# Performance work log

Hardware: AMD Instinct MI355X
Metric: run time of the kernel (lower is better)

The kernel has to match this reference:

```python
import jax, jax.numpy as jnp
import numpy as np

H, U = 64, 64  # matrix-completion patch size; system size is (H*U)^2 = 4096^2


def svtC(X, tau):
    # Singular value thresholding: soft-threshold singular values by tau.
    u, s, vt = jnp.linalg.svd(X, full_matrices=False)
    return (u * jax.nn.relu(s - tau)) @ vt


def setup_inputs() -> dict:
    key = jax.random.key(0)
    ks = jax.random.split(key, 12)
    x = jax.random.normal(ks[0], (H, U), jnp.float32)
    L = jax.random.normal(ks[1], (H, U), jnp.float32)
    entries_mask = jax.random.randint(ks[2], (H, U), 0, 2).astype(bool)
    # D_tilda: symmetric PSD (HU, HU) smoothness operator so the system is well-conditioned
    M = jax.random.normal(ks[3], (H * U, H * U), jnp.float32)
    D_tilda = (M @ M.T) / jnp.float32(H * U)
    th_P = jax.random.normal(ks[4], (H, U), jnp.float32)
    v = jax.random.normal(ks[5], (), jnp.float32)
    coef_gamma = jax.random.uniform(ks[6], (), jnp.float32)
    neta = jax.random.uniform(ks[7], (), jnp.float32)
    lamda1 = jax.random.uniform(ks[8], (), jnp.float32)
    lamda2 = jax.random.uniform(ks[9], (), jnp.float32)
    rho = jax.random.uniform(ks[10], (), jnp.float32) + jnp.float32(0.1)
    S = jax.random.normal(ks[11], (H, H), jnp.float32) / np.float32(np.sqrt(H))
    return {"x": x, "L": L, "entries_mask": entries_mask, "D_tilda": D_tilda,
            "th_P": th_P, "v": v, "coef_gamma": coef_gamma, "neta": neta,
            "lamda1": lamda1, "lamda2": lamda2, "rho": rho, "S": S}


def reference(x, L, entries_mask, D_tilda, th_P, v, coef_gamma, neta,
              lamda1, lamda2, rho, S):
    tau = jax.nn.sigmoid(v) * coef_gamma
    # Q_tilda = diag(vec(mask)); S_tilda = kron(I_U, S^T S)
    q = entries_mask.astype(jnp.float32).reshape(-1)  # (HU,)
    StS = S.T @ S                                      # (H, H)
    S_tilda = jnp.kron(jnp.eye(U, dtype=jnp.float32), StS)  # (HU, HU)
    eye = jnp.eye(H * U, dtype=jnp.float32)
    A = jnp.diag(q) + lamda1 * D_tilda + lamda2 * S_tilda + rho * eye
    vec = rho * (L - th_P) + jnp.where(entries_mask, x, jnp.float32(0.0))
    # Original uses explicit dense inverse followed by matvec
    Xtmp = (jnp.linalg.inv(A) @ vec.reshape(-1)).reshape(H, U)
    Ltmp = svtC(Xtmp + th_P, tau)
    Ptmp = th_P + neta * (Xtmp - Ltmp)
    return Ltmp, Ptmp
```

## Files before the change

### kernel.cpp

```cpp
#include <hip/hip_runtime.h>
#include <cstddef>

#define HU    4096
#define NBLK  256
#define NTHR  512
#define MAXIT 100
#define TOL2  1e-7f

#define WS_STS  0
#define WS_DINV 4096
#define WS_R0   8192
#define WS_U0   12288
#define WS_W    16384
#define WS_BAR  24576
#define WS_FLG  (WS_BAR + 1024)
#define WS_END  (WS_FLG + 128)

typedef _Float16 half4v __attribute__((ext_vector_type(4)));

__device__ __forceinline__ float fastrcp(float x) {
  float r; asm("v_rcp_f32 %0, %1" : "=v"(r) : "v"(x)); return r;
}
__device__ __forceinline__ float fastsqrt(float x) {
  float r; asm("v_sqrt_f32 %0, %1" : "=v"(r) : "v"(x)); return r;
}
__device__ __forceinline__ float fastrsq(float x) {
  float r; asm("v_rsq_f32 %0, %1" : "=v"(r) : "v"(x)); return r;
}

__device__ __forceinline__ float waveReduce(float v) {
#pragma unroll
  for (int off = 32; off > 0; off >>= 1) v += __shfl_xor(v, off, 64);
  return v;
}

__device__ __forceinline__ float blockSum(float v, float* red) {
  v = waveReduce(v);
  if ((threadIdx.x & 63) == 0) red[threadIdx.x >> 6] = v;
  __syncthreads();
  float s = 0.f;
#pragma unroll
  for (int i = 0; i < 8; ++i) s += red[i];
  __syncthreads();
  return s;
}

__device__ __forceinline__ float gsync_dk(unsigned long long* slots,
                                          unsigned long long* flgq,
                                          unsigned gen, float* red, float* dks) {
  __syncthreads();
  const int tid = threadIdx.x, lane = tid & 63, b = blockIdx.x;
  unsigned long long* arr = slots + (gen & 1) * 256;
  if (b == 0) {
    if (tid < 64) {
      if (lane == 0) {
        float s = 0.f;
#pragma unroll
        for (int i = 0; i < 8; ++i) s += red[i];
        __threadfence();
        __hip_atomic_store(&arr[0],
                           ((unsigned long long)gen << 32) | __float_as_uint(s),
                           __ATOMIC_RELEASE, __HIP_MEMORY_SCOPE_AGENT);
      }
      float dsum;
      for (;;) {
        const unsigned long long v0 = __hip_atomic_load(&arr[lane],
                                        __ATOMIC_RELAXED, __HIP_MEMORY_SCOPE_AGENT);
        const unsigned long long v1 = __hip_atomic_load(&arr[lane + 64],
                                        __ATOMIC_RELAXED, __HIP_MEMORY_SCOPE_AGENT);
        const unsigned long long v2 = __hip_atomic_load(&arr[lane + 128],
                                        __ATOMIC_RELAXED, __HIP_MEMORY_SCOPE_AGENT);
        const unsigned long long v3 = __hip_atomic_load(&arr[lane + 192],
                                        __ATOMIC_RELAXED, __HIP_MEMORY_SCOPE_AGENT);
        const bool ok = ((unsigned)(v0 >> 32) >= gen) && ((unsigned)(v1 >> 32) >= gen)
                     && ((unsigned)(v2 >> 32) >= gen) && ((unsigned)(v3 >> 32) >= gen);
        if (__all(ok)) {
          dsum = __uint_as_float((unsigned)v0) + __uint_as_float((unsigned)v1)
               + __uint_as_float((unsigned)v2) + __uint_as_float((unsigned)v3);
          break;
        }
      }
      const float dk = waveReduce(dsum);
      __threadfence();
      if (lane < 8)
        __hip_atomic_store(&flgq[lane * 8],
                           ((unsigned long long)gen << 32) | __float_as_uint(dk),
                           __ATOMIC_RELEASE, __HIP_MEMORY_SCOPE_AGENT);
      if (lane == 0) dks[0] = dk;
    }
  } else if (tid == 0) {
    float s = 0.f;
#pragma unroll
    for (int i = 0; i < 8; ++i) s += red[i];
    __threadfence();
    __hip_atomic_store(&arr[b],
                       ((unsigned long long)gen << 32) | __float_as_uint(s),
                       __ATOMIC_RELEASE, __HIP_MEMORY_SCOPE_AGENT);
    unsigned long long* fq = flgq + (b & 7) * 8;
    unsigned long long f;
    for (;;) {
      f = __hip_atomic_load(fq, __ATOMIC_RELAXED, __HIP_MEMORY_SCOPE_AGENT);
      if ((unsigned)(f >> 32) >= gen) break;
      __builtin_amdgcn_s_sleep(1);
    }
    __threadfence();
    dks[0] = __uint_as_float((unsigned)f);
  }
  __syncthreads();
  return dks[0];
}

#define SWP 6
#define S_W 68

__device__ __forceinline__ float red16(float x) {
  int t;
  t = __builtin_amdgcn_update_dpp(0, __float_as_int(x), 0x128, 0xF, 0xF, false);
  x += __int_as_float(t);
  t = __builtin_amdgcn_update_dpp(0, __float_as_int(x), 0x124, 0xF, 0xF, false);
  x += __int_as_float(t);
  t = __builtin_amdgcn_update_dpp(0, __float_as_int(x), 0x122, 0xF, 0xF, false);
  x += __int_as_float(t);
  t = __builtin_amdgcn_update_dpp(0, __float_as_int(x), 0x121, 0xF, 0xF, false);
  x += __int_as_float(t);
  return x;
}

__device__ __forceinline__ int gf8mul(int a, int b) {
  int p = 0;
  if (b & 1) p ^= a;
  if (b & 2) p ^= (a << 1);
  if (b & 4) p ^= (a << 2);
  if (p & 16) p ^= 22;
  if (p & 8)  p ^= 11;
  return p;
}

__device__ __forceinline__ int sel8(const int c[8], int i) {
  int r = c[0];
  r = (i == 1) ? c[1] : r;
  r = (i == 2) ? c[2] : r;
  r = (i == 3) ? c[3] : r;
  r = (i == 4) ? c[4] : r;
  r = (i == 5) ? c[5] : r;
  r = (i == 6) ? c[6] : r;
  r = (i == 7) ? c[7] : r;
  return r;
}

__global__ void __launch_bounds__(NTHR, 1)
fused_kernel(const float* __restrict__ x_in, const float* __restrict__ L_in,
             const int* __restrict__ mask, const float* __restrict__ D,
             const float* __restrict__ thP, const float* __restrict__ S,
             const float* __restrict__ l1p, const float* __restrict__ l2p,
             const float* __restrict__ rhop, const float* __restrict__ vp,
             const float* __restrict__ cgp, const float* __restrict__ netap,
             float* __restrict__ ws, float* __restrict__ out)
{
  __shared__ __align__(16) float u_l[HU];
  __shared__ __align__(16) char pool[128 * 1024];
  __shared__ float red[8];
  __shared__ float dks[1];
  __shared__ float g_s[64];
  __shared__ float nrm[64];
  unsigned long long* slots = (unsigned long long*)(ws + WS_BAR);
  unsigned long long* flgq  = (unsigned long long*)(ws + WS_FLG);
  const float* sts = ws + WS_STS;
  const float lam1 = *l1p, lam2 = *l2p, rho = *rhop;
  const int tid = threadIdx.x, b = blockIdx.x;
  const int wv = tid >> 6, lane = tid & 63;
  unsigned gen = 0;

  const int gtid = b * NTHR + tid;
  if (gtid < HU) {
    const int a = gtid >> 6, c = gtid & 63;
    float acc = 0.f, sdiag = 0.f;
    for (int h = 0; h < 64; ++h) {
      const float sa = S[h * 64 + a], sc = S[h * 64 + c];
      acc = fmaf(sa, sc, acc);
      sdiag = fmaf(sc, sc, sdiag);
    }
    ws[WS_STS + gtid] = acc;
    const float q = mask[gtid] ? 1.f : 0.f;
    const float diag = q + rho + lam1 * D[(size_t)gtid * (HU + 1)] + lam2 * sdiag;
    const float bb = rho * (L_in[gtid] - thP[gtid]) + (mask[gtid] ? x_in[gtid] : 0.f);
    const float di = 1.f / diag;
    ws[WS_DINV + gtid] = di;
    ws[WS_R0 + gtid] = bb;
    ws[WS_U0 + gtid] = bb * di;
  }

  {
    const float4* __restrict__ Dg = (const float4*)(D + (size_t)b * 16 * HU);
    half4v* __restrict__ Dh4 = (half4v*)pool;
    for (int o = tid; o < 16 * HU / 4; o += NTHR) {
      const float4 dv = Dg[o];
      half4v h;
      h[0] = (_Float16)dv.x; h[1] = (_Float16)dv.y;
      h[2] = (_Float16)dv.z; h[3] = (_Float16)dv.w;
      Dh4[o] = h;
    }
  }
  if (tid < 8) red[tid] = 0.f;
  gsync_dk(slots, flgq, ++gen, red, dks);

  float r_reg[8], s_reg[8], dinv_reg[8];
  float acc0 = 0.f;
#pragma unroll
  for (int m = 0; m < 8; ++m) {
    const int i = tid + m * NTHR;
    const float rv = ws[WS_R0 + i], uv = ws[WS_U0 + i];
    r_reg[m] = rv; u_l[i] = uv; dinv_reg[m] = ws[WS_DINV + i];
    s_reg[m] = 0.f;
  }
  __syncthreads();
#pragma unroll
  for (int m = 0; m < 8; ++m) acc0 = fmaf(r_reg[m], u_l[tid + m * NTHR], acc0);
  const float gamma0 = blockSum(acc0, red);

  float p_arr[8], x_arr[8];
#pragma unroll
  for (int m = 0; m < 8; ++m) { p_arr[m] = 0.f; x_arr[m] = 0.f; }

  const int row0 = b * 16 + wv * 2;
  const int iq = row0 >> 6, j0 = row0 & 63;
  const float4* __restrict__ u4 = (const float4*)u_l;
  const float m0 = mask[row0] ? 1.f : 0.f;
  const float m1 = mask[row0 + 1] ? 1.f : 0.f;
  const float sts0 = sts[j0 * 64 + lane];
  const float sts1 = sts[j0 * 64 + 64 + lane];
  const float dex0 = D[(size_t)row0 * (HU + 1)];
  const float dex1 = D[(size_t)(row0 + 1) * (HU + 1)];
  const float diagf0 = m0 + rho + lam1 * (dex0 - (float)(_Float16)dex0);
  const float diagf1 = m1 + rho + lam1 * (dex1 - (float)(_Float16)dex1);
  const half4v* __restrict__ H0 = (const half4v*)((_Float16*)pool + (size_t)(wv * 2) * HU);
  const half4v* __restrict__ H1 = H0 + (HU / 4);

  float gamma = gamma0, gamma_prev = 1.f, alpha_prev = 1.f;
  for (int k = 0; k < MAXIT; ++k) {
    float* __restrict__ wbuf = ws + WS_W + (k & 1) * HU;
    {
      float acc_a = 0.f, acc_b = 0.f;
#pragma unroll
      for (int it = 0; it < 16; ++it) {
        const float4 uu = u4[it * 64 + lane];
        const half4v d0 = H0[it * 64 + lane];
        const half4v d1 = H1[it * 64 + lane];
        acc_a = fmaf((float)d0[0], uu.x, acc_a); acc_a = fmaf((float)d0[1], uu.y, acc_a);
        acc_a = fmaf((float)d0[2], uu.z, acc_a); acc_a = fmaf((float)d0[3], uu.w, acc_a);
        acc_b = fmaf((float)d1[0], uu.x, acc_b); acc_b = fmaf((float)d1[1], uu.y, acc_b);
        acc_b = fmaf((float)d1[2], uu.z, acc_b); acc_b = fmaf((float)d1[3], uu.w, acc_b);
      }
      const float us = u_l[iq * 64 + lane];
      float t0 = fmaf(lam1, acc_a, lam2 * (sts0 * us));
      float t1 = fmaf(lam1, acc_b, lam2 * (sts1 * us));
      t0 = waveReduce(t0);
      t1 = waveReduce(t1);
      const float u0v = u_l[row0], u1v = u_l[row0 + 1];
      const float w0 = t0 + diagf0 * u0v;
      const float w1 = t1 + diagf1 * u1v;
      if (lane == 0) {
        wbuf[row0] = w0;
        wbuf[row0 + 1] = w1;
        red[wv] = fmaf(w0, u0v, w1 * u1v);
      }
    }
    const float dk = gsync_dk(slots, flgq, ++gen, red, dks);

    float wv_r[8];
#pragma unroll
    for (int m = 0; m < 8; ++m) wv_r[m] = wbuf[tid + m * NTHR];

    const float beta  = (k == 0) ? 0.f : gamma * fastrcp(gamma_prev);
    const float denom = (k == 0) ? dk  : (dk - beta * gamma * fastrcp(alpha_prev));
    const float alpha = gamma * fastrcp(denom);

    float acc = 0.f;
#pragma unroll
    for (int m = 0; m < 8; ++m) {
      const int i = tid + m * NTHR;
      const float uold = u_l[i];
      const float sv = (k == 0) ? wv_r[m] : fmaf(beta, s_reg[m], wv_r[m]);
      s_reg[m] = sv;
      const float rv = fmaf(-alpha, sv, r_reg[m]);
      r_reg[m] = rv;
      const float uv = rv * dinv_reg[m];
      u_l[i] = uv;
      acc = fmaf(rv, uv, acc);
      if (b == 0) {
        const float pk = (k == 0) ? uold : fmaf(beta, p_arr[m], uold);
        p_arr[m] = pk;
        x_arr[m] = fmaf(alpha, pk, x_arr[m]);
      }
    }
    const float gnext = blockSum(acc, red);

    gamma_prev = gamma;
    alpha_prev = alpha;
    gamma = gnext;
    if (!(gnext > TOL2 * gamma0)) break;
  }

  if (b != 0) return;

  float* Wl = (float*)pool;
  float* Yr = Wl + 64 * S_W;
  float* T1 = Yr + 64 * S_W;
  float* Wr = T1 + 64 * S_W;
  __syncthreads();

  float t0acc = 0.f;
#pragma unroll
  for (int mm = 0; mm < 8; ++mm) {
    const int i = tid + mm * NTHR;
    const int rr = i >> 6, cc = i & 63;
    const float y = x_arr[mm] + thP[i];
    Wl[cc * S_W + rr] = y;
    Yr[rr * S_W + cc] = y;
    t0acc = fmaf(y, y, t0acc);
  }
  const float T0 = blockSum(t0acc, red);
  if (tid < 64) {
    const float4* wc = (const float4*)(Wl + tid * S_W);
    float nn = 0.f;
#pragma unroll
    for (int i2 = 0; i2 < 16; ++i2) {
      const float4 u = wc[i2];
      nn = fmaf(u.x, u.x, fmaf(u.y, u.y, fmaf(u.z, u.z, fmaf(u.w, u.w, nn))));
    }
    nrm[tid] = nn;
  }
  __syncthreads();
  const float thr = 1.6e-7f * T0 * T0;

  const int team = lane >> 4;
  const int sub  = lane & 15;

  for (int sweep = 0; sweep < SWP; ++sweep) {
    float offacc = 0.f;
#pragma unroll
    for (int mr = 0; mr < 9; ++mr) {
      int cols[8];
#pragma unroll
      for (int j = 0; j < 8; ++j)
        cols[j] = (mr == 8) ? (8 * wv + j) : (8 * j + (gf8mul(mr, j) ^ wv));
      for (int r = 0; r < 7; ++r) {
        const int pi = (team == 0) ? 7 : ((r + team) % 7);
        const int qi = (team == 0) ? (r % 7) : ((r + 7 - team) % 7);
        const int cp = sel8(cols, pi);
        const int cq = sel8(cols, qi);
        float4* wp = (float4*)(Wl + cp * S_W) + sub;
        float4* wq = (float4*)(Wl + cq * S_W) + sub;
        const float4 a = *wp, bb = *wq;
        const float dpp = nrm[cp];
        const float dqq = nrm[cq];
        float dpq = fmaf(a.x, bb.x, fmaf(a.y, bb.y, fmaf(a.z, bb.z, a.w * bb.w)));
        dpq = red16(dpq);
        offacc = fmaf(dpq, dpq, offacc);
        if (dpq * dpq > 1e-14f * dpp * dqq) {
          const float d  = dqq - dpp;
          const float u2 = 2.f * dpq;
          const float z  = fmaf(d, d, u2 * u2);
          const float ih = fastrsq(z);
          const float c1 = fastsqrt(fmaf(0.5f * fabsf(d), ih, 0.5f));
          const float sg = (d >= 0.f) ? 0.5f : -0.5f;
          const float s1 = sg * u2 * ih * fastrcp(c1);
          float4 na, nb;
          na.x = c1 * a.x - s1 * bb.x;  nb.x = s1 * a.x + c1 * bb.x;
          na.y = c1 * a.y - s1 * bb.y;  nb.y = s1 * a.y + c1 * bb.y;
          na.z = c1 * a.z - s1 * bb.z;  nb.z = s1 * a.z + c1 * bb.z;
          na.w = c1 * a.w - s1 * bb.w;  nb.w = s1 * a.w + c1 * bb.w;
          *wp = na; *wq = nb;
          if (sub == 0) {
            const float cc2 = c1 * c1, ss2 = s1 * s1, cs2 = 2.f * c1 * s1;
            nrm[cp] = cc2 * dpp - cs2 * dpq + ss2 * dqq;
            nrm[cq] = ss2 * dpp + cs2 * dpq + cc2 * dqq;
          }
        }
      }
      __syncthreads();
    }
    const float tot = blockSum(offacc, red);
    if (tot < thr) break;
  }

  if (tid < 64) {
    const float4* wc = (const float4*)(Wl + tid * S_W);
    float nn = 0.f;
#pragma unroll
    for (int i2 = 0; i2 < 16; ++i2) {
      const float4 u = wc[i2];
      nn = fmaf(u.x, u.x, fmaf(u.y, u.y, fmaf(u.z, u.z, fmaf(u.w, u.w, nn))));
    }
    const float sv = sqrtf(nn);
    const float tau = (*cgp) / (1.f + expf(-(*vp)));
    g_s[tid] = (sv > tau) ? (sv - tau) / (sv * nn) : 0.f;
  }
  __syncthreads();

  const int j = tid & 63;
  const int ib = tid >> 6;

#pragma unroll
  for (int mm = 0; mm < 8; ++mm) {
    const int k = ib + 8 * mm;
    const float4* wcol = (const float4*)(Wl + k * S_W);
    float acc = 0.f;
#pragma unroll
    for (int i4 = 0; i4 < 16; ++i4) {
      const float4 wvv = wcol[i4];
      acc = fmaf(wvv.x, Yr[(4 * i4 + 0) * S_W + j], acc);
      acc = fmaf(wvv.y, Yr[(4 * i4 + 1) * S_W + j], acc);
      acc = fmaf(wvv.z, Yr[(4 * i4 + 2) * S_W + j], acc);
      acc = fmaf(wvv.w, Yr[(4 * i4 + 3) * S_W + j], acc);
    }
    T1[k * S_W + j] = acc;
  }
  for (int o = tid; o < 4096; o += 512) {
    const int i2 = o >> 6, kk = o & 63;
    Wr[i2 * S_W + kk] = Wl[kk * S_W + i2] * g_s[kk];
  }
  __syncthreads();

  const float neta = *netap;
#pragma unroll
  for (int mm = 0; mm < 8; ++mm) {
    const int i2 = ib + 8 * mm;
    const float4* wrow = (const float4*)(Wr + i2 * S_W);
    float acc = 0.f;
#pragma unroll
    for (int k4 = 0; k4 < 16; ++k4) {
      const float4 wvv = wrow[k4];
      acc = fmaf(wvv.x, T1[(4 * k4 + 0) * S_W + j], acc);
      acc = fmaf(wvv.y, T1[(4 * k4 + 1) * S_W + j], acc);
      acc = fmaf(wvv.z, T1[(4 * k4 + 2) * S_W + j], acc);
      acc = fmaf(wvv.w, T1[(4 * k4 + 3) * S_W + j], acc);
    }
    const int o = i2 * 64 + j;
    out[o] = acc;
    out[4096 + o] = thP[o] + neta * (x_arr[mm] - acc);
  }
}

extern "C" void kernel_launch(void* const* d_in, const int* in_sizes, int n_in,
                              void* d_out, int out_size, void* d_ws, size_t ws_size,
                              hipStream_t stream)
{
  const float* x_in  = (const float*)d_in[0];
  const float* L_in  = (const float*)d_in[1];
  const int*   mask  = (const int*)d_in[2];
  const float* D     = (const float*)d_in[3];
  const float* thP   = (const float*)d_in[4];
  const float* vp    = (const float*)d_in[5];
  const float* cgp   = (const float*)d_in[6];
  const float* netap = (const float*)d_in[7];
  const float* l1p   = (const float*)d_in[8];
  const float* l2p   = (const float*)d_in[9];
  const float* rhop  = (const float*)d_in[10];
  const float* S     = (const float*)d_in[11];
  float* ws  = (float*)d_ws;
  float* out = (float*)d_out;

  hipMemsetAsync(ws + WS_BAR, 0, (WS_END - WS_BAR) * sizeof(float), stream);

  void* args[] = { (void*)&x_in, (void*)&L_in, (void*)&mask, (void*)&D, (void*)&thP,
                   (void*)&S, (void*)&l1p, (void*)&l2p, (void*)&rhop,
                   (void*)&vp, (void*)&cgp, (void*)&netap, (void*)&ws, (void*)&out };
  hipLaunchCooperativeKernel((void*)fused_kernel, dim3(NBLK), dim3(NTHR),
                             args, 0, stream);
}
```

Before: 317.2 us.

## Keep Jacobi SVD column blocks in registers and rotate whole columns per wave

The one-sided Jacobi sweep used to split each wave into four 16-lane teams, each rotating one column pair through float4 LDS loads and stores. Now each wave loads its 8 columns into registers once per round (one element per lane), does all 7 rotation steps on them with full 64-lane reductions for the four pairs at a time, and writes the columns and norms back at the end. This removes repeated LDS traffic and the dynamic index selection, at the cost of more shuffle reductions. The convergence threshold is also loosened fourfold, so the sweep loop can exit earlier, which may slightly change accuracy.

```diff
diff --git a/kernel.cpp b/kernel.cpp
--- a/kernel.cpp
+++ b/kernel.cpp
@@ -126,6 +126,13 @@
   return x;
 }
 
+__device__ __forceinline__ float reduce64(float x) {
+  x = red16(x);
+  x += __shfl_xor(x, 16, 64);
+  x += __shfl_xor(x, 32, 64);
+  return x;
+}
+
 __device__ __forceinline__ int gf8mul(int a, int b) {
   int p = 0;
   if (b & 1) p ^= a;
@@ -134,18 +141,6 @@
   if (p & 16) p ^= 22;
   if (p & 8)  p ^= 11;
   return p;
-}
-
-__device__ __forceinline__ int sel8(const int c[8], int i) {
-  int r = c[0];
-  r = (i == 1) ? c[1] : r;
-  r = (i == 2) ? c[2] : r;
-  r = (i == 3) ? c[3] : r;
-  r = (i == 4) ? c[4] : r;
-  r = (i == 5) ? c[5] : r;
-  r = (i == 6) ? c[6] : r;
-  r = (i == 7) ? c[7] : r;
-  return r;
 }
 
 __global__ void __launch_bounds__(NTHR, 1)
@@ -331,52 +326,66 @@
     nrm[tid] = nn;
   }
   __syncthreads();
-  const float thr = 1.6e-7f * T0 * T0;
-
-  const int team = lane >> 4;
-  const int sub  = lane & 15;
+  const float thr = 6.4e-7f * T0 * T0;
 
   for (int sweep = 0; sweep < SWP; ++sweep) {
     float offacc = 0.f;
-#pragma unroll
     for (int mr = 0; mr < 9; ++mr) {
       int cols[8];
 #pragma unroll
       for (int j = 0; j < 8; ++j)
         cols[j] = (mr == 8) ? (8 * wv + j) : (8 * j + (gf8mul(mr, j) ^ wv));
+      float w[8], n[8];
+#pragma unroll
+      for (int j = 0; j < 8; ++j) {
+        w[j] = Wl[cols[j] * S_W + lane];
+        n[j] = nrm[cols[j]];
+      }
+#pragma unroll
       for (int r = 0; r < 7; ++r) {
-        const int pi = (team == 0) ? 7 : ((r + team) % 7);
-        const int qi = (team == 0) ? (r % 7) : ((r + 7 - team) % 7);
-        const int cp = sel8(cols, pi);
-        const int cq = sel8(cols, qi);
-        float4* wp = (float4*)(Wl + cp * S_W) + sub;
-        float4* wq = (float4*)(Wl + cq * S_W) + sub;
-        const float4 a = *wp, bb = *wq;
-        const float dpp = nrm[cp];
-        const float dqq = nrm[cq];
-        float dpq = fmaf(a.x, bb.x, fmaf(a.y, bb.y, fmaf(a.z, bb.z, a.w * bb.w)));
-        dpq = red16(dpq);
-        offacc = fmaf(dpq, dpq, offacc);
-        if (dpq * dpq > 1e-14f * dpp * dqq) {
-          const float d  = dqq - dpp;
-          const float u2 = 2.f * dpq;
-          const float z  = fmaf(d, d, u2 * u2);
-          const float ih = fastrsq(z);
-          const float c1 = fastsqrt(fmaf(0.5f * fabsf(d), ih, 0.5f));
-          const float sg = (d >= 0.f) ? 0.5f : -0.5f;
-          const float s1 = sg * u2 * ih * fastrcp(c1);
-          float4 na, nb;
-          na.x = c1 * a.x - s1 * bb.x;  nb.x = s1 * a.x + c1 * bb.x;
-          na.y = c1 * a.y - s1 * bb.y;  nb.y = s1 * a.y + c1 * bb.y;
-          na.z = c1 * a.z - s1 * bb.z;  nb.z = s1 * a.z + c1 * bb.z;
-          na.w = c1 * a.w - s1 * bb.w;  nb.w = s1 * a.w + c1 * bb.w;
-          *wp = na; *wq = nb;
-          if (sub == 0) {
-            const float cc2 = c1 * c1, ss2 = s1 * s1, cs2 = 2.f * c1 * s1;
-            nrm[cp] = cc2 * dpp - cs2 * dpq + ss2 * dqq;
-            nrm[cq] = ss2 * dpp + cs2 * dpq + cc2 * dqq;
-          }
+        const int P0 = 7,           Q0 = r % 7;
+        const int P1 = (r + 1) % 7, Q1 = (r + 6) % 7;
+        const int P2 = (r + 2) % 7, Q2 = (r + 5) % 7;
+        const int P3 = (r + 3) % 7, Q3 = (r + 4) % 7;
+        float d0 = reduce64(w[P0] * w[Q0]);
+        float d1 = reduce64(w[P1] * w[Q1]);
+        float d2 = reduce64(w[P2] * w[Q2]);
+        float d3 = reduce64(w[P3] * w[Q3]);
+        offacc = fmaf(d0, d0, offacc);
+        offacc = fmaf(d1, d1, offacc);
+        offacc = fmaf(d2, d2, offacc);
+        offacc = fmaf(d3, d3, offacc);
+#define ROTPAIR(PI, QI, DPQ)                                                   \
+        {                                                                      \
+          const float dpp = n[PI], dqq = n[QI];                                \
+          if (DPQ * DPQ > 1e-14f * dpp * dqq) {       \
+            const float d  = dqq - dpp;                                        \
+            const float u2 = 2.f * DPQ;                                        \
+            const float z  = fmaf(d, d, u2 * u2);                              \
+            const float ih = fastrsq(z);                                       \
+            const float c1 = fastsqrt(fmaf(0.5f * fabsf(d), ih, 0.5f));        \
+            const float sg = (d >= 0.f) ? 0.5f : -0.5f;                        \
+            const float s1 = sg * u2 * ih * fastrcp(c1);                       \
+            const float wp = w[PI], wq = w[QI];                                \
+            w[PI] = c1 * wp - s1 * wq;                                         \
+            w[QI] = s1 * wp + c1 * wq;                                         \
+            const float cc2 = c1 * c1, ss2 = s1 * s1, cs2 = 2.f * c1 * s1;     \
+            n[PI] = cc2 * dpp - cs2 * DPQ + ss2 * dqq;                         \
+            n[QI] = ss2 * dpp + cs2 * DPQ + cc2 * dqq;                         \
+          }                                                                    \
         }
+        ROTPAIR(P0, Q0, d0)
+        ROTPAIR(P1, Q1, d1)
+        ROTPAIR(P2, Q2, d2)
+        ROTPAIR(P3, Q3, d3)
+#undef ROTPAIR
+      }
+#pragma unroll
+      for (int j = 0; j < 8; ++j)
+        Wl[cols[j] * S_W + lane] = w[j];
+      if (lane == 0) {
+#pragma unroll
+        for (int j = 0; j < 8; ++j) nrm[cols[j]] = n[j];
       }
       __syncthreads();
     }
```

Measured after the change: 716.9 us. 2.26x slower.
